# Kernel optimization log

Measured on AMD Instinct MI355X. Metric: run time of the kernel, lower is better.

Reference implementation:

```python
import jax, jax.numpy as jnp
import numpy as np

B, NQ, NK, D = 64, 1024, 1024, 128
MASK_VALUE = -1e6


def setup_inputs() -> dict:
    key = jax.random.key(0)
    kq, kk, kv, kl = jax.random.split(key, 4)
    queries = jax.random.normal(kq, (B, NQ, D), dtype=jnp.float32)
    keys = jax.random.normal(kk, (B, NK, D), dtype=jnp.float32)
    values = jax.random.normal(kv, (B, NK, D), dtype=jnp.float32)
    valid_lens = jax.random.randint(kl, (B,), 1, NK + 1, dtype=jnp.int32)
    return {"queries": queries, "keys": keys, "values": values, "valid_lens": valid_lens}


def reference(queries, keys, values, valid_lens):
    d = queries.shape[-1]
    # scores: [B, Nq, Nk]
    scores = jnp.einsum("bqd,bkd->bqk", queries, keys) / jnp.sqrt(jnp.float32(d))
    # valid_lens [B] -> mask over last (key) axis, same for every query row
    key_pos = jnp.arange(scores.shape[-1])  # [Nk]
    mask = key_pos[None, None, :] < valid_lens[:, None, None]  # [B,1,Nk] broadcast
    scores = jnp.where(mask, scores, jnp.float32(MASK_VALUE))
    attn = jax.nn.softmax(scores, axis=-1)
    # dropout p=0.0 (eval): identity
    return jnp.einsum("bqk,bkd->bqd", attn, values)
```

## Files before the change

kernel.cpp:

```cpp
#include <hip/hip_runtime.h>

typedef __bf16 bf16x8 __attribute__((ext_vector_type(8)));
typedef __bf16 bf16x4 __attribute__((ext_vector_type(4)));
typedef float f32x4 __attribute__((ext_vector_type(4)));

namespace {
constexpr int kNQ = 1024;
constexpr int kNK = 1024;
constexpr int kD = 128;
constexpr int kBQ = 64;
constexpr int kBK = 32;
constexpr int kKStride = 136;
constexpr int kVStride = 32;
constexpr int kPStride = 40;
constexpr float kScaleLog2e = 0.12751742f;
}

__global__ void lpt_sort(const int* __restrict__ VL, int* __restrict__ perm) {
    const int t = threadIdx.x;
    const int v = VL[t];
    int rank = 0;
    for (int j = 0; j < 64; ++j) {
        const int vj = VL[j];
        rank += (vj > v) || (vj == v && j < t);
    }
    perm[rank] = t;
}

__global__ __launch_bounds__(256, 4)
void fa_fwd(const float* __restrict__ Q, const float* __restrict__ K,
            const float* __restrict__ V, const int* __restrict__ VL,
            const int* __restrict__ perm, float* __restrict__ O)
{
    __shared__ __align__(16) __bf16 kls[2][kBK * kKStride];
    __shared__ __align__(16) __bf16 vls[2][kD * kVStride];
    __shared__ __align__(16) __bf16 pls[4 * 16 * kPStride];

    const int tid  = threadIdx.x;
    const int wave = tid >> 6;
    const int lane = tid & 63;
    const int quad = lane >> 4;
    const int c16  = lane & 15;

    const int b    = perm[blockIdx.x >> 4];
    const int qblk = blockIdx.x & 15;
    const int q0   = qblk * kBQ + wave * 16;

    const int valid  = VL[b];
    const int ntiles = (valid + kBK - 1) / kBK;

    bf16x8 qf[4];
    {
        const float* qp = Q + ((size_t)b * kNQ + q0 + c16) * kD + quad * 8;
        #pragma unroll
        for (int f = 0; f < 4; ++f) {
            #pragma unroll
            for (int j = 0; j < 8; ++j) qf[f][j] = (__bf16)qp[f * 32 + j];
        }
    }

    bf16x8 ones;
    #pragma unroll
    for (int j = 0; j < 8; ++j) ones[j] = (__bf16)1.0f;

    f32x4 acc[9];
    #pragma unroll
    for (int f = 0; f < 9; ++f) {
        acc[f][0] = 0.f; acc[f][1] = 0.f; acc[f][2] = 0.f; acc[f][3] = 0.f;
    }

    const int ksrow = tid >> 3;
    const int kscol = (tid & 7) * 16;
    const int vkg   = (tid & 7) * 4;
    const int vdb   = (tid >> 3) * 4;

    f32x4 kr[4], vr[4];

    auto load_regs = [&](int kbase) {
        const float* kp = K + ((size_t)b * kNK + kbase + ksrow) * kD + kscol;
        #pragma unroll
        for (int i = 0; i < 4; ++i) kr[i] = *(const f32x4*)(kp + i * 4);
        const float* vp = V + ((size_t)b * kNK + kbase + vkg) * kD + vdb;
        #pragma unroll
        for (int i = 0; i < 4; ++i) vr[i] = *(const f32x4*)(vp + (size_t)i * kD);
    };

    auto cvt_write = [&](int bufi) {
        bf16x8 kh;
        #pragma unroll
        for (int j = 0; j < 8; ++j) kh[j] = (__bf16)kr[j >> 2][j & 3];
        *(bf16x8*)&kls[bufi][ksrow * kKStride + kscol] = kh;
        #pragma unroll
        for (int j = 0; j < 8; ++j) kh[j] = (__bf16)kr[2 + (j >> 2)][j & 3];
        *(bf16x8*)&kls[bufi][ksrow * kKStride + kscol + 8] = kh;
        #pragma unroll
        for (int j = 0; j < 4; ++j) {
            bf16x4 vh;
            #pragma unroll
            for (int i = 0; i < 4; ++i) vh[i] = (__bf16)vr[i][j];
            *(bf16x4*)&vls[bufi][(vdb + j) * kVStride + vkg] = vh;
        }
    };

    load_regs(0);
    cvt_write(0);
    __syncthreads();

    int cur = 0;
    for (int t = 0; t < ntiles; ++t) {
        const int kb = t * kBK;
        const bool more = (t + 1 < ntiles);
        if (more) load_regs(kb + kBK);

        f32x4 s0 = {0.f, 0.f, 0.f, 0.f};
        f32x4 s1 = {0.f, 0.f, 0.f, 0.f};
        const __bf16* kbuf = kls[cur];
        #pragma unroll
        for (int f = 0; f < 4; ++f) {
            bf16x8 kf = *(const bf16x8*)&kbuf[c16 * kKStride + f * 32 + quad * 8];
            s0 = __builtin_amdgcn_mfma_f32_16x16x32_bf16(qf[f], kf, s0, 0, 0, 0);
        }
        #pragma unroll
        for (int f = 0; f < 4; ++f) {
            bf16x8 kf = *(const bf16x8*)&kbuf[(16 + c16) * kKStride + f * 32 + quad * 8];
            s1 = __builtin_amdgcn_mfma_f32_16x16x32_bf16(qf[f], kf, s1, 0, 0, 0);
        }

        if (kb + kBK > valid) {
            if (kb + c16 >= valid) {
                #pragma unroll
                for (int r = 0; r < 4; ++r) s0[r] = -1e30f;
            }
            if (kb + 16 + c16 >= valid) {
                #pragma unroll
                for (int r = 0; r < 4; ++r) s1[r] = -1e30f;
            }
        }

        #pragma unroll
        for (int r = 0; r < 4; ++r) {
            s0[r] = exp2f(s0[r] * kScaleLog2e);
            s1[r] = exp2f(s1[r] * kScaleLog2e);
        }

        {
            __bf16* pb = &pls[wave * 16 * kPStride];
            #pragma unroll
            for (int r = 0; r < 4; ++r) {
                pb[(quad * 4 + r) * kPStride + c16]      = (__bf16)s0[r];
                pb[(quad * 4 + r) * kPStride + 16 + c16] = (__bf16)s1[r];
            }
        }
        const bf16x8 pf =
            *(const bf16x8*)&pls[(wave * 16 + c16) * kPStride + quad * 8];

        const __bf16* vbuf = vls[cur];
        #pragma unroll
        for (int f = 0; f < 8; ++f) {
            const bf16x8 vf = *(const bf16x8*)&vbuf[(f * 16 + c16) * kVStride + quad * 8];
            acc[f] = __builtin_amdgcn_mfma_f32_16x16x32_bf16(pf, vf, acc[f], 0, 0, 0);
        }
        acc[8] = __builtin_amdgcn_mfma_f32_16x16x32_bf16(pf, ones, acc[8], 0, 0, 0);

        if (more) cvt_write(cur ^ 1);
        __syncthreads();
        cur ^= 1;
    }

    float* ob = O + ((size_t)b * kNQ + q0) * kD;
    #pragma unroll
    for (int r = 0; r < 4; ++r) {
        const float inv = 1.0f / acc[8][r];
        #pragma unroll
        for (int f = 0; f < 8; ++f) {
            ob[(quad * 4 + r) * kD + f * 16 + c16] = acc[f][r] * inv;
        }
    }
}

extern "C" void kernel_launch(void* const* d_in, const int* in_sizes, int n_in,
                              void* d_out, int out_size, void* d_ws, size_t ws_size,
                              hipStream_t stream) {
    const float* Q = (const float*)d_in[0];
    const float* K = (const float*)d_in[1];
    const float* V = (const float*)d_in[2];
    const int*  VL = (const int*)d_in[3];
    float* O = (float*)d_out;
    int* perm = (int*)d_ws;
    lpt_sort<<<1, 64, 0, stream>>>(VL, perm);
    fa_fwd<<<dim3(64 * 16), 256, 0, stream>>>(Q, K, V, VL, perm, O);
}
```

Measured before the change: 187.2 us.

## Transpose QK^T MFMA and move P to A-operand via bpermute instead of LDS

Swaps the QK^T MFMA operands so each lane holds key-indexed scores, then builds the P fragment for the PV MFMA through ds_bpermute lane shuffles instead of a round trip through a per-wave shared-memory scratch buffer. The mask is recomputed per accumulator row to match the transposed layout. The score accumulation is split into two independent chains to shorten the MFMA dependency, and the next tile's LDS write is moved before the PV MFMAs to overlap with them. This adds eight bpermutes and selects per tile and relies on the lane mapping being correct.

```diff
diff --git a/kernel.cpp b/kernel.cpp
--- a/kernel.cpp
+++ b/kernel.cpp
@@ -2,7 +2,9 @@
 
 typedef __bf16 bf16x8 __attribute__((ext_vector_type(8)));
 typedef __bf16 bf16x4 __attribute__((ext_vector_type(4)));
+typedef __bf16 bf16x2 __attribute__((ext_vector_type(2)));
 typedef float f32x4 __attribute__((ext_vector_type(4)));
+typedef int i32x4 __attribute__((ext_vector_type(4)));
 
 namespace {
 constexpr int kNQ = 1024;
@@ -12,8 +14,12 @@
 constexpr int kBK = 32;
 constexpr int kKStride = 136;
 constexpr int kVStride = 32;
-constexpr int kPStride = 40;
 constexpr float kScaleLog2e = 0.12751742f;
+}
+
+__device__ __forceinline__ int packbf(float a, float b) {
+    bf16x2 t; t[0] = (__bf16)a; t[1] = (__bf16)b;
+    return __builtin_bit_cast(int, t);
 }
 
 __global__ void lpt_sort(const int* __restrict__ VL, int* __restrict__ perm) {
@@ -34,7 +40,6 @@
 {
     __shared__ __align__(16) __bf16 kls[2][kBK * kKStride];
     __shared__ __align__(16) __bf16 vls[2][kD * kVStride];
-    __shared__ __align__(16) __bf16 pls[4 * 16 * kPStride];
 
     const int tid  = threadIdx.x;
     const int wave = tid >> 6;
@@ -102,6 +107,9 @@
         }
     };
 
+    const int a0 = ((quad & 1) << 7) + (c16 << 2);
+    const int a1 = a0 + 64;
+
     load_regs(0);
     cvt_write(0);
     __syncthreads();
@@ -112,28 +120,37 @@
         const bool more = (t + 1 < ntiles);
         if (more) load_regs(kb + kBK);
 
-        f32x4 s0 = {0.f, 0.f, 0.f, 0.f};
-        f32x4 s1 = {0.f, 0.f, 0.f, 0.f};
+        f32x4 s0a = {0.f,0.f,0.f,0.f}, s0b = {0.f,0.f,0.f,0.f};
+        f32x4 s1a = {0.f,0.f,0.f,0.f}, s1b = {0.f,0.f,0.f,0.f};
         const __bf16* kbuf = kls[cur];
         #pragma unroll
-        for (int f = 0; f < 4; ++f) {
+        for (int f = 0; f < 2; ++f) {
             bf16x8 kf = *(const bf16x8*)&kbuf[c16 * kKStride + f * 32 + quad * 8];
-            s0 = __builtin_amdgcn_mfma_f32_16x16x32_bf16(qf[f], kf, s0, 0, 0, 0);
-        }
-        #pragma unroll
-        for (int f = 0; f < 4; ++f) {
+            s0a = __builtin_amdgcn_mfma_f32_16x16x32_bf16(kf, qf[f], s0a, 0, 0, 0);
+        }
+        #pragma unroll
+        for (int f = 2; f < 4; ++f) {
+            bf16x8 kf = *(const bf16x8*)&kbuf[c16 * kKStride + f * 32 + quad * 8];
+            s0b = __builtin_amdgcn_mfma_f32_16x16x32_bf16(kf, qf[f], s0b, 0, 0, 0);
+        }
+        #pragma unroll
+        for (int f = 0; f < 2; ++f) {
             bf16x8 kf = *(const bf16x8*)&kbuf[(16 + c16) * kKStride + f * 32 + quad * 8];
-            s1 = __builtin_amdgcn_mfma_f32_16x16x32_bf16(qf[f], kf, s1, 0, 0, 0);
-        }
+            s1a = __builtin_amdgcn_mfma_f32_16x16x32_bf16(kf, qf[f], s1a, 0, 0, 0);
+        }
+        #pragma unroll
+        for (int f = 2; f < 4; ++f) {
+            bf16x8 kf = *(const bf16x8*)&kbuf[(16 + c16) * kKStride + f * 32 + quad * 8];
+            s1b = __builtin_amdgcn_mfma_f32_16x16x32_bf16(kf, qf[f], s1b, 0, 0, 0);
+        }
+        f32x4 s0 = s0a + s0b;
+        f32x4 s1 = s1a + s1b;
 
         if (kb + kBK > valid) {
-            if (kb + c16 >= valid) {
-                #pragma unroll
-                for (int r = 0; r < 4; ++r) s0[r] = -1e30f;
-            }
-            if (kb + 16 + c16 >= valid) {
-                #pragma unroll
-                for (int r = 0; r < 4; ++r) s1[r] = -1e30f;
+            #pragma unroll
+            for (int r = 0; r < 4; ++r) {
+                if (kb + quad * 4 + r >= valid)      s0[r] = -1e30f;
+                if (kb + 16 + quad * 4 + r >= valid) s1[r] = -1e30f;
             }
         }
 
@@ -143,16 +160,25 @@
             s1[r] = exp2f(s1[r] * kScaleLog2e);
         }
 
-        {
-            __bf16* pb = &pls[wave * 16 * kPStride];
-            #pragma unroll
-            for (int r = 0; r < 4; ++r) {
-                pb[(quad * 4 + r) * kPStride + c16]      = (__bf16)s0[r];
-                pb[(quad * 4 + r) * kPStride + 16 + c16] = (__bf16)s1[r];
-            }
-        }
-        const bf16x8 pf =
-            *(const bf16x8*)&pls[(wave * 16 + c16) * kPStride + quad * 8];
+        const int pp01 = packbf(s0[0], s0[1]), pp23 = packbf(s0[2], s0[3]);
+        const int qq01 = packbf(s1[0], s1[1]), qq23 = packbf(s1[2], s1[3]);
+        const int b0p = __builtin_amdgcn_ds_bpermute(a0, pp01);
+        const int b0q = __builtin_amdgcn_ds_bpermute(a0, qq01);
+        const int b1p = __builtin_amdgcn_ds_bpermute(a0, pp23);
+        const int b1q = __builtin_amdgcn_ds_bpermute(a0, qq23);
+        const int b2p = __builtin_amdgcn_ds_bpermute(a1, pp01);
+        const int b2q = __builtin_amdgcn_ds_bpermute(a1, qq01);
+        const int b3p = __builtin_amdgcn_ds_bpermute(a1, pp23);
+        const int b3q = __builtin_amdgcn_ds_bpermute(a1, qq23);
+        const bool lo = quad < 2;
+        i32x4 pd;
+        pd[0] = lo ? b0p : b0q;
+        pd[1] = lo ? b1p : b1q;
+        pd[2] = lo ? b2p : b2q;
+        pd[3] = lo ? b3p : b3q;
+        const bf16x8 pf = __builtin_bit_cast(bf16x8, pd);
+
+        if (more) cvt_write(cur ^ 1);
 
         const __bf16* vbuf = vls[cur];
         #pragma unroll
@@ -162,7 +188,6 @@
         }
         acc[8] = __builtin_amdgcn_mfma_f32_16x16x32_bf16(pf, ones, acc[8], 0, 0, 0);
 
-        if (more) cvt_write(cur ^ 1);
         __syncthreads();
         cur ^= 1;
     }
```

Result: no change. 183.9 us (-1.8%).
